# Performance work log

Measured on AMD Instinct MI355X. Metric: run time of the kernel, lower is better.

## Reference

```python
import jax, jax.numpy as jnp
import numpy as np

B, N, D, F = 4, 50000, 8, 128

def setup_inputs() -> dict:
    key = jax.random.key(0)
    ks = jax.random.split(key, 6)
    x = jax.random.normal(ks[0], (B, N, F), dtype=jnp.float32)
    adj = jax.random.randint(ks[1], (N, D), 0, N, dtype=jnp.int32)
    # torch.nn.Linear weights: [out_features, in_features], in = 2*F
    W1 = jax.random.normal(ks[2], (F, 2 * F), dtype=jnp.float32) * 0.05
    b1 = jax.random.normal(ks[3], (F,), dtype=jnp.float32) * 0.05
    W2 = jax.random.normal(ks[4], (F, 2 * F), dtype=jnp.float32) * 0.05
    b2 = jax.random.normal(ks[5], (F,), dtype=jnp.float32) * 0.05
    return {"x": x, "adj": adj, "W1": W1, "b1": b1, "W2": W2, "b2": b2}

def _gnn_layer(x, adj, W, b):
    # x: [B, N, F]; adj: [N, D]
    nb = x[:, adj, :]                 # [B, N, D, F] irregular gather
    agg = jnp.max(nb, axis=2)         # max-aggregate over neighbors -> [B, N, F]
    cc = jnp.concatenate([agg, x], axis=-1)  # [B, N, 2F]
    return jax.nn.relu(jnp.einsum('bnf,of->bno', cc, W) + b)

def reference(x, adj, W1, b1, W2, b2):
    x = _gnn_layer(x, adj, W1, b1)
    x = _gnn_layer(x, adj, W2, b2)
    return x
```

## Files before the change

kernel.cpp:

```cpp
#include <hip/hip_runtime.h>


#define N_NODES 50000
#define N_BATCH 4
#define DEG 8
#define FDIM 128
#define K2 256
#define TILE_N 16

typedef _Float16 f16x8 __attribute__((ext_vector_type(8)));
typedef _Float16 f16x4 __attribute__((ext_vector_type(4)));
typedef float f32x4 __attribute__((ext_vector_type(4)));

__global__ void split_w_kernel(const float* __restrict__ W1, const float* __restrict__ W2,
                               _Float16* __restrict__ w1h, _Float16* __restrict__ w1l,
                               _Float16* __restrict__ w2h, _Float16* __restrict__ w2l) {
  const int i = blockIdx.x * 256 + threadIdx.x;
  {
    const float a = W1[i];
    const _Float16 h = (_Float16)a;
    w1h[i] = h;
    w1l[i] = (_Float16)(a - (float)h);
  }
  {
    const float a = W2[i];
    const _Float16 h = (_Float16)a;
    w2h[i] = h;
    w2l[i] = (_Float16)(a - (float)h);
  }
}

__global__ void transpose_x_kernel(const float* __restrict__ x, _Float16* __restrict__ xT) {
  const int wv = threadIdx.x >> 6, l = threadIdx.x & 63;
  const int n = blockIdx.x * 4 + wv;
  const int b = l >> 4;
  const int c8 = (l & 15) * 8;
  const float* src = x + ((size_t)b * N_NODES + n) * FDIM + c8;
  const f32x4 v0 = *(const f32x4*)src;
  const f32x4 v1 = *(const f32x4*)(src + 4);
  f16x8 h;
  #pragma unroll
  for (int j = 0; j < 4; ++j) h[j] = (_Float16)v0[j];
  #pragma unroll
  for (int j = 0; j < 4; ++j) h[4 + j] = (_Float16)v1[j];
  *(f16x8*)(xT + ((size_t)n * N_BATCH + b) * FDIM + c8) = h;
}

static __device__ inline f16x8 vmax8(f16x8 a, f16x8 b) {
  f16x8 r;
  #pragma unroll
  for (int j = 0; j < 8; ++j) r[j] = a[j] > b[j] ? a[j] : b[j];
  return r;
}

template <bool OUT_F32>
__global__ __launch_bounds__(256, 5)
void gnn_layer_kernel(const _Float16* __restrict__ xT, const int* __restrict__ adj,
                      const _Float16* __restrict__ Wh, const _Float16* __restrict__ Wl,
                      const float* __restrict__ bias, void* __restrict__ out_) {
  __shared__ unsigned char lds[32768];

  const int tid = (int)threadIdx.x;
  const int n0  = (int)blockIdx.x * TILE_N;

  const int l   = tid & 63;
  const int wv  = tid >> 6;
  const int col = l & 15;
  const int kg  = l >> 4;
  const int o0  = wv * 32;

  const int bb = l >> 4;
  const int c8 = (l & 15) * 8;
  #pragma unroll 2
  for (int i = 0; i < 4; ++i) {
    const int nl = wv * 4 + i;
    const int ng = n0 + nl;
    const int* arow = adj + ng * DEG;
    const size_t laneoff = (size_t)bb * FDIM + c8;
    f16x8 v[DEG];
    #pragma unroll
    for (int d = 0; d < DEG; ++d)
      v[d] = *(const f16x8*)(xT + (size_t)arow[d] * (N_BATCH * FDIM) + laneoff);
    const f16x8 xv = *(const f16x8*)(xT + (size_t)ng * (N_BATCH * FDIM) + laneoff);
    const f16x8 agg = vmax8(vmax8(vmax8(v[0], v[1]), vmax8(v[2], v[3])),
                            vmax8(vmax8(v[4], v[5]), vmax8(v[6], v[7])));
    const int r   = nl * N_BATCH + bb;
    const int swz = (r & 7) << 4;
    *(f16x8*)(lds + r * 512 + ((c8 * 2) ^ swz))       = agg;
    *(f16x8*)(lds + r * 512 + (256 + ((c8 * 2) ^ swz))) = xv;
  }

  __syncthreads();

  f32x4 acc[4][2] = {};
  #pragma unroll
  for (int h2 = 0; h2 < 2; ++h2) {
    #pragma unroll
    for (int kt = 0; kt < 4; ++kt) {
      const int k = h2 * 128 + kt * 32 + kg * 8;
      const f16x8 Bh0 = *(const f16x8*)(Wh + (o0 + col) * K2 + k);
      const f16x8 Bh1 = *(const f16x8*)(Wh + (o0 + 16 + col) * K2 + k);
      const f16x8 Bl0 = *(const f16x8*)(Wl + (o0 + col) * K2 + k);
      const f16x8 Bl1 = *(const f16x8*)(Wl + (o0 + 16 + col) * K2 + k);
      f16x8 Ah[4];
      #pragma unroll
      for (int mf = 0; mf < 4; ++mf) {
        const int row = mf * 16 + col;
        const int kb  = k * 2;
        Ah[mf] = *(const f16x8*)(lds + row * 512 +
                                 ((kb & 256) | ((kb & 255) ^ ((row & 7) << 4))));
      }
      #pragma unroll
      for (int mf = 0; mf < 4; ++mf) {
        acc[mf][0] = __builtin_amdgcn_mfma_f32_16x16x32_f16(Ah[mf], Bh0, acc[mf][0], 0, 0, 0);
        acc[mf][0] = __builtin_amdgcn_mfma_f32_16x16x32_f16(Ah[mf], Bl0, acc[mf][0], 0, 0, 0);
        acc[mf][1] = __builtin_amdgcn_mfma_f32_16x16x32_f16(Ah[mf], Bh1, acc[mf][1], 0, 0, 0);
        acc[mf][1] = __builtin_amdgcn_mfma_f32_16x16x32_f16(Ah[mf], Bl1, acc[mf][1], 0, 0, 0);
      }
    }
  }

  const float bv0 = bias[o0 + col];
  const float bv1 = bias[o0 + 16 + col];
  #pragma unroll
  for (int mf = 0; mf < 4; ++mf) {
    #pragma unroll
    for (int j = 0; j < 4; ++j) {
      const int r = mf * 16 + kg * 4 + j;
      const float r0 = fmaxf(acc[mf][0][j] + bv0, 0.f);
      const float r1 = fmaxf(acc[mf][1][j] + bv1, 0.f);
      if (OUT_F32) {
        const int b = r & 3, n = n0 + (r >> 2);
        float* orow = (float*)out_ + ((size_t)b * N_NODES + n) * FDIM;
        __builtin_nontemporal_store(r0, &orow[o0 + col]);
        __builtin_nontemporal_store(r1, &orow[o0 + 16 + col]);
      } else {
        _Float16* orow = (_Float16*)out_ + ((size_t)n0 * N_BATCH + r) * FDIM;
        orow[o0 + col]      = (_Float16)r0;
        orow[o0 + 16 + col] = (_Float16)r1;
      }
    }
  }
}

extern "C" void kernel_launch(void* const* d_in, const int* in_sizes, int n_in,
                              void* d_out, int out_size, void* d_ws, size_t ws_size,
                              hipStream_t stream) {
  const float* x  = (const float*)d_in[0];
  const int* adj  = (const int*)d_in[1];
  const float* W1 = (const float*)d_in[2];
  const float* b1 = (const float*)d_in[3];
  const float* W2 = (const float*)d_in[4];
  const float* b2 = (const float*)d_in[5];
  float* out      = (float*)d_out;

  char* ws = (char*)d_ws;
  const size_t nElem = (size_t)N_BATCH * N_NODES * FDIM;
  _Float16* xT    = (_Float16*)ws;
  _Float16* inter = xT + nElem;
  _Float16* w1h   = inter + nElem;
  _Float16* w1l   = w1h + 32768;
  _Float16* w2h   = w1l + 32768;
  _Float16* w2l   = w2h + 32768;

  split_w_kernel<<<128, 256, 0, stream>>>(W1, W2, w1h, w1l, w2h, w2l);
  transpose_x_kernel<<<12500, 256, 0, stream>>>(x, xT);

  const int grid = N_NODES / TILE_N;
  gnn_layer_kernel<false><<<grid, 256, 0, stream>>>(xT, adj, w1h, w1l, b1, inter);
  gnn_layer_kernel<true><<<grid, 256, 0, stream>>>(inter, adj, w2h, w2l, b2, out);
}
```

Before: 363.1 us.

## Halve node tile, raise occupancy, and load adjacency as scalar indices

Cuts the node tile from 16 to 8 per block, halving LDS to 16KB and the MFMA accumulator set, and raises the launch-bounds occupancy hint from 5 to 8. Adjacency indices for both nodes a wave handles are loaded up front with vector int4 loads and moved into scalar registers via readfirstlane. Together these aim to keep more gathers in flight to hide irregular memory latency. In exchange, each block reloads the full weight fragments for half as many rows, doubling per-node weight traffic from cache.

```diff
diff --git a/kernel.cpp b/kernel.cpp
--- a/kernel.cpp
+++ b/kernel.cpp
@@ -6,7 +6,7 @@
 #define DEG 8
 #define FDIM 128
 #define K2 256
-#define TILE_N 16
+#define TILE_N 8
 
 typedef _Float16 f16x8 __attribute__((ext_vector_type(8)));
 typedef _Float16 f16x4 __attribute__((ext_vector_type(4)));
@@ -54,11 +54,11 @@
 }
 
 template <bool OUT_F32>
-__global__ __launch_bounds__(256, 5)
+__global__ __launch_bounds__(256, 8)
 void gnn_layer_kernel(const _Float16* __restrict__ xT, const int* __restrict__ adj,
                       const _Float16* __restrict__ Wh, const _Float16* __restrict__ Wl,
                       const float* __restrict__ bias, void* __restrict__ out_) {
-  __shared__ unsigned char lds[32768];
+  __shared__ unsigned char lds[16384];
 
   const int tid = (int)threadIdx.x;
   const int n0  = (int)blockIdx.x * TILE_N;
@@ -71,28 +71,50 @@
 
   const int bb = l >> 4;
   const int c8 = (l & 15) * 8;
-  #pragma unroll 2
-  for (int i = 0; i < 4; ++i) {
-    const int nl = wv * 4 + i;
-    const int ng = n0 + nl;
-    const int* arow = adj + ng * DEG;
-    const size_t laneoff = (size_t)bb * FDIM + c8;
+  const size_t laneoff = (size_t)bb * FDIM + c8;
+
+  const int nbase = n0 + wv * 2;
+  int idx[2][8];
+  {
+    const int4* ap4 = (const int4*)(adj + nbase * DEG);
+    const int4 q0 = ap4[0], q1 = ap4[1], q2 = ap4[2], q3 = ap4[3];
+    idx[0][0] = __builtin_amdgcn_readfirstlane(q0.x);
+    idx[0][1] = __builtin_amdgcn_readfirstlane(q0.y);
+    idx[0][2] = __builtin_amdgcn_readfirstlane(q0.z);
+    idx[0][3] = __builtin_amdgcn_readfirstlane(q0.w);
+    idx[0][4] = __builtin_amdgcn_readfirstlane(q1.x);
+    idx[0][5] = __builtin_amdgcn_readfirstlane(q1.y);
+    idx[0][6] = __builtin_amdgcn_readfirstlane(q1.z);
+    idx[0][7] = __builtin_amdgcn_readfirstlane(q1.w);
+    idx[1][0] = __builtin_amdgcn_readfirstlane(q2.x);
+    idx[1][1] = __builtin_amdgcn_readfirstlane(q2.y);
+    idx[1][2] = __builtin_amdgcn_readfirstlane(q2.z);
+    idx[1][3] = __builtin_amdgcn_readfirstlane(q2.w);
+    idx[1][4] = __builtin_amdgcn_readfirstlane(q3.x);
+    idx[1][5] = __builtin_amdgcn_readfirstlane(q3.y);
+    idx[1][6] = __builtin_amdgcn_readfirstlane(q3.z);
+    idx[1][7] = __builtin_amdgcn_readfirstlane(q3.w);
+  }
+
+  #pragma unroll
+  for (int i = 0; i < 2; ++i) {
+    const int ng = nbase + i;
     f16x8 v[DEG];
     #pragma unroll
     for (int d = 0; d < DEG; ++d)
-      v[d] = *(const f16x8*)(xT + (size_t)arow[d] * (N_BATCH * FDIM) + laneoff);
+      v[d] = *(const f16x8*)(xT + (size_t)idx[i][d] * (N_BATCH * FDIM) + laneoff);
     const f16x8 xv = *(const f16x8*)(xT + (size_t)ng * (N_BATCH * FDIM) + laneoff);
     const f16x8 agg = vmax8(vmax8(vmax8(v[0], v[1]), vmax8(v[2], v[3])),
                             vmax8(vmax8(v[4], v[5]), vmax8(v[6], v[7])));
-    const int r   = nl * N_BATCH + bb;
+    const int r   = (wv * 2 + i) * N_BATCH + bb;
     const int swz = (r & 7) << 4;
-    *(f16x8*)(lds + r * 512 + ((c8 * 2) ^ swz))       = agg;
+    *(f16x8*)(lds + r * 512 + ((c8 * 2) ^ swz))         = agg;
     *(f16x8*)(lds + r * 512 + (256 + ((c8 * 2) ^ swz))) = xv;
   }
 
   __syncthreads();
 
-  f32x4 acc[4][2] = {};
+  f32x4 acc[2][2] = {};
   #pragma unroll
   for (int h2 = 0; h2 < 2; ++h2) {
     #pragma unroll
@@ -102,16 +124,16 @@
       const f16x8 Bh1 = *(const f16x8*)(Wh + (o0 + 16 + col) * K2 + k);
       const f16x8 Bl0 = *(const f16x8*)(Wl + (o0 + col) * K2 + k);
       const f16x8 Bl1 = *(const f16x8*)(Wl + (o0 + 16 + col) * K2 + k);
-      f16x8 Ah[4];
+      f16x8 Ah[2];
       #pragma unroll
-      for (int mf = 0; mf < 4; ++mf) {
+      for (int mf = 0; mf < 2; ++mf) {
         const int row = mf * 16 + col;
         const int kb  = k * 2;
         Ah[mf] = *(const f16x8*)(lds + row * 512 +
                                  ((kb & 256) | ((kb & 255) ^ ((row & 7) << 4))));
       }
       #pragma unroll
-      for (int mf = 0; mf < 4; ++mf) {
+      for (int mf = 0; mf < 2; ++mf) {
         acc[mf][0] = __builtin_amdgcn_mfma_f32_16x16x32_f16(Ah[mf], Bh0, acc[mf][0], 0, 0, 0);
         acc[mf][0] = __builtin_amdgcn_mfma_f32_16x16x32_f16(Ah[mf], Bl0, acc[mf][0], 0, 0, 0);
         acc[mf][1] = __builtin_amdgcn_mfma_f32_16x16x32_f16(Ah[mf], Bh1, acc[mf][1], 0, 0, 0);
@@ -123,7 +145,7 @@
   const float bv0 = bias[o0 + col];
   const float bv1 = bias[o0 + 16 + col];
   #pragma unroll
-  for (int mf = 0; mf < 4; ++mf) {
+  for (int mf = 0; mf < 2; ++mf) {
     #pragma unroll
     for (int j = 0; j < 4; ++j) {
       const int r = mf * 16 + kg * 4 + j;
```

Measured after the change: 410.9 us. 1.13x slower.
